# Kernel tuning notes

Hardware: AMD Instinct MI355X
Metric: run time of the kernel (lower is better)

The kernel has to match this reference:

```python
import jax, jax.numpy as jnp
import numpy as np
from jax import lax

B, H, W = 8, 96, 160
CF = 64        # feature channels (= input_channels//2 = out_channels)
OC = 64        # out channels
K = 3          # kernel
G = 8          # deform (offset) groups
PAD, DIL = 1, 1


def conv3x3(x, w, b):
    y = lax.conv_general_dilated(x, w, (1, 1), ((PAD, PAD), (PAD, PAD)),
                                 dimension_numbers=('NCHW', 'OIHW', 'NCHW'))
    return y + b[None, :, None, None]


def lrelu(x):
    return jnp.where(x >= 0, x, 0.1 * x)


def deform_conv2d(x, offset, mask, w, b):
    # x: (B, Cin, H, W); offset: (B, 2*G*K*K, H, W) in (y, x) per tap; mask: (B, G*K*K, H, W)
    Bq, Cin, Hq, Wq = x.shape
    OCq = w.shape[0]
    off = offset.reshape(Bq, G, K, K, 2, Hq, Wq)
    dy, dx = off[:, :, :, :, 0], off[:, :, :, :, 1]        # (B,G,K,K,H,W)
    ky = jnp.arange(K, dtype=x.dtype).reshape(1, 1, K, 1, 1, 1)
    kx = jnp.arange(K, dtype=x.dtype).reshape(1, 1, 1, K, 1, 1)
    hy = jnp.arange(Hq, dtype=x.dtype).reshape(1, 1, 1, 1, Hq, 1)
    wx = jnp.arange(Wq, dtype=x.dtype).reshape(1, 1, 1, 1, 1, Wq)
    ys = dy + hy - PAD + ky * DIL                          # sampling rows
    xs = dx + wx - PAAD if False else dx + wx - PAD + kx * DIL  # sampling cols
    xg = x.reshape(Bq, G, Cin // G, Hq, Wq)

    def sample(img, ysg, xsg):
        # img: (Cg,H,W); ysg/xsg: (K,K,H,W) -> (Cg,K,K,H,W) bilinear with zero padding
        y0 = jnp.floor(ysg)
        x0 = jnp.floor(xsg)
        wy1 = ysg - y0
        wx1 = xsg - x0
        wy0 = 1.0 - wy1
        wx0 = 1.0 - wx1

        def gather(yi, xi):
            valid = ((yi >= 0) & (yi < Hq) & (xi >= 0) & (xi < Wq)).astype(img.dtype)
            yc = jnp.clip(yi, 0, Hq - 1).astype(jnp.int32)
            xc = jnp.clip(xi, 0, Wq - 1).astype(jnp.int32)
            return img[:, yc, xc] * valid[None]

        return (gather(y0, x0) * (wy0 * wx0)[None]
                + gather(y0, x0 + 1) * (wy0 * wx1)[None]
                + gather(y0 + 1, x0) * (wy1 * wx0)[None]
                + gather(y0 + 1, x0 + 1) * (wy1 * wx1)[None])

    sampled = jax.vmap(jax.vmap(sample))(xg, ys, xs)       # (B,G,Cg,K,K,H,W)
    sampled = sampled * mask.reshape(Bq, G, 1, K, K, Hq, Wq)
    wg = w.reshape(OCq, G, Cin // G, K, K)
    return jnp.einsum('bgcijhw,ogcij->bohw', sampled, wg) + b[None, :, None, None]


def setup_inputs() -> dict:
    key = jax.random.key(0)
    ks = jax.random.split(key, 12)
    cin0 = OC * 3 + 4  # 196

    def u(k, shape, fan_in):
        s = 1.0 / np.sqrt(fan_in)
        return jax.random.uniform(k, shape, jnp.float32, -s, s)

    inp = {
        'current_feature_warped': jax.random.normal(ks[0], (B, CF, H, W), jnp.float32),
        'feat_prop': jax.random.normal(ks[1], (B, CF, H, W), jnp.float32),
        'feat_prev': jax.random.normal(ks[2], (B, CF, H, W), jnp.float32),
        'flow1': jax.random.normal(ks[3], (B, 2, H, W), jnp.float32),
        'flow2': jax.random.normal(ks[4], (B, 2, H, W), jnp.float32),
        'w1': u(ks[5], (OC, cin0, 3, 3), cin0 * 9), 'b1': jnp.zeros((OC,), jnp.float32),
        'w2': u(ks[6], (OC, OC, 3, 3), OC * 9), 'b2': jnp.zeros((OC,), jnp.float32),
        'w3': u(ks[7], (OC, OC, 3, 3), OC * 9), 'b3': jnp.zeros((OC,), jnp.float32),
        'w4': u(ks[8], (K * K * 3 * G, OC, 3, 3), OC * 9), 'b4': jnp.zeros((K * K * 3 * G,), jnp.float32),
        'weight': u(ks[9], (OC, CF, 3, 3), 128 * 9),  # init_weights uses n = input_channels*k*k = 128*9
        'bias': jnp.zeros((OC,), jnp.float32),
    }
    return inp

# remove the accidental typo guard (keeps module exec-clean)
PAAD = PAD


def reference(current_feature_warped, feat_prop, feat_prev, flow1, flow2,
              w1, b1, w2, b2, w3, b3, w4, b4, weight, bias):
    cat = jnp.concatenate([current_feature_warped, feat_prop, feat_prev, flow1, flow2], axis=1)
    o = lrelu(conv3x3(cat, w1, b1))
    o = lrelu(conv3x3(o, w2, b2))
    o = lrelu(conv3x3(o, w3, b3))
    o = conv3x3(o, w4, b4)                                  # (B, 3*G*K*K, H, W)
    offset1, offset2, mask = jnp.split(o, 3, axis=1)        # each (B, G*K*K, H, W)
    rep = offset1.shape[1] // 2                             # G*K*K/2 = 36
    offset1 = offset1 + jnp.tile(flow1[:, ::-1], (1, rep, 1, 1))
    offset2 = offset2 + jnp.tile(flow2[:, ::-1], (1, rep, 1, 1))
    offset = jnp.concatenate([offset1, offset2], axis=1)    # (B, 2*G*K*K, H, W)
    mask = jax.nn.sigmoid(mask)
    return deform_conv2d(current_feature_warped, offset, mask, weight, bias)
```

## Files before the change

kernel.cpp:

```cpp
#include <hip/hip_runtime.h>
#include <hip/hip_bf16.h>
#include <math.h>

typedef __attribute__((ext_vector_type(8))) short short8;
typedef __attribute__((ext_vector_type(4))) float f32x4;

constexpr int B_ = 8, H_ = 96, W_ = 160;
constexpr int HW_ = H_ * W_;
constexpr int NPIX = B_ * HW_;

__device__ __forceinline__ unsigned short f2bf(float f) {
    unsigned int u = __builtin_bit_cast(unsigned int, f);
    u += 0x7FFFu + ((u >> 16) & 1u);
    return (unsigned short)(u >> 16);
}
__device__ __forceinline__ float bf2f(unsigned short s) {
    unsigned int u = ((unsigned int)s) << 16;
    return __builtin_bit_cast(float, u);
}
__device__ __forceinline__ unsigned int cvt_pk_bf16(float lo, float hi) {
    unsigned int r;
    asm volatile("v_cvt_pk_bf16_f32 %0, %1, %2" : "=v"(r) : "v"(lo), "v"(hi));
    return r;
}
__device__ __forceinline__ float f4get(const float4& v, int q) {
    switch (q) { case 0: return v.x; case 1: return v.y;
                 case 2: return v.z; default: return v.w; }
}

__global__ __launch_bounds__(256) void prep_x1(
    const float* __restrict__ cfw, const float* __restrict__ fpro,
    const float* __restrict__ fprv, const float* __restrict__ f1,
    const float* __restrict__ f2, unsigned short* __restrict__ X1)
{
    const int c8 = blockIdx.y;
    const int pix0 = blockIdx.x * 1024 + threadIdx.x * 4;
    unsigned short* dst = X1 + ((size_t)c8 * NPIX + pix0) * 8;

    if (c8 >= 25) {
        uint4 z = {0u, 0u, 0u, 0u};
        #pragma unroll
        for (int q = 0; q < 4; ++q) *(uint4*)(dst + q * 8) = z;
        return;
    }

    const int b  = pix0 / HW_;
    const int hw = pix0 - b * HW_;

    float4 v[8];
    #pragma unroll
    for (int j = 0; j < 8; ++j) {
        int c = c8 * 8 + j;
        const float* src = nullptr; int sc = 0, nc = 0;
        if (c < 64)       { src = cfw;  sc = c;       nc = 64; }
        else if (c < 128) { src = fpro; sc = c - 64;  nc = 64; }
        else if (c < 192) { src = fprv; sc = c - 128; nc = 64; }
        else if (c < 194) { src = f1;   sc = c - 192; nc = 2;  }
        else if (c < 196) { src = f2;   sc = c - 194; nc = 2;  }
        if (src) v[j] = *(const float4*)(src + ((size_t)b * nc + sc) * HW_ + hw);
        else     { v[j].x = v[j].y = v[j].z = v[j].w = 0.f; }
    }
    #pragma unroll
    for (int q = 0; q < 4; ++q) {
        uint4 o;
        o.x = cvt_pk_bf16(f4get(v[0], q), f4get(v[1], q));
        o.y = cvt_pk_bf16(f4get(v[2], q), f4get(v[3], q));
        o.z = cvt_pk_bf16(f4get(v[4], q), f4get(v[5], q));
        o.w = cvt_pk_bf16(f4get(v[6], q), f4get(v[7], q));
        *(uint4*)(dst + q * 8) = o;
    }
}

__global__ __launch_bounds__(256) void prep_w(
    const float* __restrict__ w, unsigned short* __restrict__ Bt,
    int Cin, int KCH, int Nout, int NFTOT)
{
    int idx = blockIdx.x * 256 + threadIdx.x;
    int total = 9 * KCH * NFTOT * 64;
    if (idx >= total) return;
    int lane = idx & 63;
    int r = idx >> 6;
    int nf = r % NFTOT; r /= NFTOT;
    int ck = r % KCH;
    int t  = r / KCH;
    int n  = nf * 16 + (lane & 15);
    int kb = ck * 32 + (lane >> 4) * 8;
    short8 o;
    #pragma unroll
    for (int j = 0; j < 8; ++j) {
        int c = kb + j;
        float v = (c < Cin && n < Nout) ? w[((size_t)n * Cin + c) * 9 + t] : 0.f;
        o[j] = (short)f2bf(v);
    }
    *(short8*)(Bt + (size_t)idx * 8) = o;
}

__global__ __launch_bounds__(256) void prep_wd(
    const float* __restrict__ w, unsigned short* __restrict__ Btd)
{
    int idx = blockIdx.x * 256 + threadIdx.x;
    if (idx >= 8 * 3 * 4 * 64) return;
    int lane = idx & 63;
    int r = idx >> 6;
    int nf = r % 4; r >>= 2;
    int ck = r % 3;
    int g  = r / 3;
    int n  = nf * 16 + (lane & 15);
    int kb = ck * 32 + (lane >> 4) * 8;
    short8 o;
    #pragma unroll
    for (int j = 0; j < 8; ++j) {
        int k = kb + j;
        int t = k >> 3, c = k & 7;
        float v = (t < 9) ? w[((size_t)n * 64 + g * 8 + c) * 9 + t] : 0.f;
        o[j] = (short)f2bf(v);
    }
    *(short8*)(Btd + (size_t)idx * 8) = o;
}

template<int KCH, int NFTOT, int NF, bool RELU>
__global__ __launch_bounds__(256) void conv_mfma(
    const unsigned short* __restrict__ X, const unsigned short* __restrict__ Bt,
    const float* __restrict__ bias, unsigned short* __restrict__ Y,
    int CoutTot, int fBase0)
{
    const int lane = threadIdx.x & 63;
    const int wv   = threadIdx.x >> 6;
    const int m0   = blockIdx.x * 128 + wv * 32;
    const int fBase = fBase0 + blockIdx.y * NF;
    const int lm = lane & 15;
    const int l16 = lane >> 4;

    int p[2], hh[2], wp[2];
    #pragma unroll
    for (int mf = 0; mf < 2; ++mf) {
        int pm = m0 + mf * 16 + lm;
        p[mf] = pm;
        hh[mf] = (pm / W_) % H_;
        wp[mf] = pm % W_;
    }

    f32x4 acc[2][NF];
    #pragma unroll
    for (int nf = 0; nf < NF; ++nf) {
        int oc = (fBase + nf) * 16 + lm;
        float bv = (oc < CoutTot) ? bias[oc] : 0.f;
        f32x4 a = {bv, bv, bv, bv};
        acc[0][nf] = a; acc[1][nf] = a;
    }

    const short8 zero = {0,0,0,0,0,0,0,0};

    #pragma unroll
    for (int ck = 0; ck < KCH; ++ck) {
        const int p8 = ck * 4 + l16;
        const unsigned short* Xp = X + (size_t)p8 * NPIX * 8;
        #pragma unroll
        for (int t = 0; t < 9; ++t) {
            const int di = t / 3 - 1, dj = t % 3 - 1;
            const unsigned short* bp =
                Bt + (((size_t)(t * KCH + ck) * NFTOT + fBase) * 64 + lane) * 8;
            short8 bfr[NF];
            #pragma unroll
            for (int nf = 0; nf < NF; ++nf)
                bfr[nf] = *(const short8*)(bp + (size_t)nf * 512);
            #pragma unroll
            for (int mf = 0; mf < 2; ++mf) {
                bool val = ((unsigned)(hh[mf] + di) < (unsigned)H_) &&
                           ((unsigned)(wp[mf] + dj) < (unsigned)W_);
                const unsigned short* ap = Xp + (size_t)(p[mf] + di * W_ + dj) * 8;
                short8 afr = val ? *(const short8*)ap : zero;
                #pragma unroll
                for (int nf = 0; nf < NF; ++nf)
                    acc[mf][nf] = __builtin_amdgcn_mfma_f32_16x16x32_bf16(
                        afr, bfr[nf], acc[mf][nf], 0, 0, 0);
            }
        }
    }

    const int prow = l16 * 4;
    #pragma unroll
    for (int mf = 0; mf < 2; ++mf)
        #pragma unroll
        for (int nf = 0; nf < NF; ++nf) {
            int oc = (fBase + nf) * 16 + lm;
            if (oc < CoutTot) {
                #pragma unroll
                for (int r = 0; r < 4; ++r) {
                    int pix = m0 + mf * 16 + prow + r;
                    float v = acc[mf][nf][r];
                    if (RELU) v = (v >= 0.f) ? v : 0.1f * v;
                    Y[((size_t)(oc >> 3) * NPIX + pix) * 8 + (oc & 7)] = f2bf(v);
                }
            }
        }
}

template<int HALF>
__global__ __launch_bounds__(256, 4) void conv4_mfma(
    const unsigned short* __restrict__ X, const unsigned short* __restrict__ Bt,
    const float* __restrict__ bias,
    unsigned short* __restrict__ oY, unsigned short* __restrict__ oX,
    unsigned short* __restrict__ oM)
{
    const int lane = threadIdx.x & 63;
    const int wv   = threadIdx.x >> 6;
    const int pix0 = blockIdx.x * 128;
    const int m0   = pix0 + wv * 32;
    const int lm = lane & 15;
    const int l16 = lane >> 4;
    constexpr int FB = HALF * 7;

    int p[2], hh[2], wp[2];
    #pragma unroll
    for (int mf = 0; mf < 2; ++mf) {
        int pm = m0 + mf * 16 + lm;
        p[mf] = pm;
        hh[mf] = (pm / W_) % H_;
        wp[mf] = pm % W_;
    }

    f32x4 acc[2][7];
    #pragma unroll
    for (int nf = 0; nf < 7; ++nf) {
        int oc = (FB + nf) * 16 + lm;
        float bv = (oc < 216) ? bias[oc] : 0.f;
        f32x4 a = {bv, bv, bv, bv};
        acc[0][nf] = a; acc[1][nf] = a;
    }

    const short8 zero = {0,0,0,0,0,0,0,0};

    #pragma unroll
    for (int ck = 0; ck < 2; ++ck) {
        const unsigned short* Xp = X + (size_t)(ck * 4 + l16) * NPIX * 8;
        #pragma unroll
        for (int t = 0; t < 9; ++t) {
            const int di = t / 3 - 1, dj = t % 3 - 1;
            const unsigned short* bp =
                Bt + (((size_t)(t * 2 + ck) * 14 + FB) * 64 + lane) * 8;
            short8 afr[2];
            #pragma unroll
            for (int mf = 0; mf < 2; ++mf) {
                bool val = ((unsigned)(hh[mf] + di) < (unsigned)H_) &&
                           ((unsigned)(wp[mf] + dj) < (unsigned)W_);
                const unsigned short* ap = Xp + (size_t)(p[mf] + di * W_ + dj) * 8;
                afr[mf] = val ? *(const short8*)ap : zero;
            }
            #pragma unroll
            for (int nf = 0; nf < 7; ++nf) {
                short8 bfr = *(const short8*)(bp + (size_t)nf * 512);
                acc[0][nf] = __builtin_amdgcn_mfma_f32_16x16x32_bf16(
                    afr[0], bfr, acc[0][nf], 0, 0, 0);
                acc[1][nf] = __builtin_amdgcn_mfma_f32_16x16x32_bf16(
                    afr[1], bfr, acc[1][nf], 0, 0, 0);
            }
        }
    }

    const int prow = l16 * 4;
    #pragma unroll
    for (int mf = 0; mf < 2; ++mf) {
        const int pixb = m0 + mf * 16 + prow;
        #pragma unroll
        for (int nf = 0; nf < 7; ++nf) {
            const int nfg = FB + nf;
            const int oc = nfg * 16 + lm;
            if (nfg < 9) {
                const int pr = nfg * 8 + (lm >> 1);
                unsigned short* plane = ((lm & 1) ? oX : oY) + (size_t)pr * NPIX;
                uint2 sv;
                sv.x = cvt_pk_bf16(acc[mf][nf][0], acc[mf][nf][1]);
                sv.y = cvt_pk_bf16(acc[mf][nf][2], acc[mf][nf][3]);
                *(uint2*)(plane + pixb) = sv;
            } else if (oc < 216) {
                const int mi = (nfg - 9) * 16 + lm;
                float v0 = 1.f / (1.f + expf(-acc[mf][nf][0]));
                float v1 = 1.f / (1.f + expf(-acc[mf][nf][1]));
                float v2 = 1.f / (1.f + expf(-acc[mf][nf][2]));
                float v3 = 1.f / (1.f + expf(-acc[mf][nf][3]));
                uint2 sv;
                sv.x = cvt_pk_bf16(v0, v1);
                sv.y = cvt_pk_bf16(v2, v3);
                *(uint2*)(oM + (size_t)mi * NPIX + pixb) = sv;
            }
        }
    }
}

__global__ __launch_bounds__(256) void deform_mfma(
    const unsigned short* __restrict__ Xg,
    const unsigned short* __restrict__ oY,
    const unsigned short* __restrict__ oX,
    const unsigned short* __restrict__ oM,
    const float* __restrict__ f1, const float* __restrict__ f2,
    const unsigned short* __restrict__ Btd,
    const float* __restrict__ bia,
    float* __restrict__ out)
{
    __shared__ __align__(16) char lds[128 * 65 * 4];
    float* sout = (float*)lds;

    const int tid  = threadIdx.x;
    const int lane = tid & 63;
    const int wv   = tid >> 6;
    const int lm   = lane & 15;
    const int pix0 = blockIdx.x * 128;
    const int b    = pix0 / HW_;
    const int hw0  = pix0 % HW_;

    const int pix = tid & 127;
    const int hi  = tid >> 7;
    const int hw  = hw0 + pix;
    const int h   = hw / W_;
    const int w   = hw - h * W_;
    const size_t gp = (size_t)(pix0 + pix);
    const size_t bF = (size_t)b * 2 * HW_;

    {
        uint4 z = {0u, 0u, 0u, 0u};
        #pragma unroll
        for (int i = 0; i < 8; ++i)
            ((uint4*)lds)[i * 256 + tid] = z;
    }

    f32x4 acc[2][4];
    #pragma unroll
    for (int nf = 0; nf < 4; ++nf) {
        float bv = bia[nf * 16 + lm];
        f32x4 a = {bv, bv, bv, bv};
        acc[0][nf] = a; acc[1][nf] = a;
    }

    for (int g = 0; g < 8; ++g) {
        const unsigned short* Xp = Xg + (size_t)g * NPIX * 8;
        __syncthreads();

        const float* fl = (g < 4) ? f1 : f2;
        const float fy = fl[bF + (size_t)HW_ + hw];
        const float fx = fl[bF + hw];
        unsigned short uy[5], ux[5], um[5];
        #pragma unroll
        for (int it = 0; it < 5; ++it) {
            int t = hi + 2 * it;
            bool act = (it < 4) || (hi == 0);
            if (act) {
                size_t po = (size_t)(g * 9 + t) * NPIX + gp;
                uy[it] = oY[po]; ux[it] = oX[po]; um[it] = oM[po];
            }
        }
        #pragma unroll
        for (int it = 0; it < 5; ++it) {
            int t = hi + 2 * it;
            bool act = (it < 4) || (hi == 0);
            if (act) {
                float dy = bf2f(uy[it]) + fy;
                float dx = bf2f(ux[it]) + fx;
                float m  = bf2f(um[it]);

                float ys = dy + (float)(h - 1 + t / 3);
                float xs = dx + (float)(w - 1 + t % 3);
                float y0f = floorf(ys), x0f = floorf(xs);
                float wy1 = ys - y0f, wx1 = xs - x0f;
                float wy0 = 1.f - wy1, wx0 = 1.f - wx1;
                int iy0 = (int)y0f, ix0 = (int)x0f;
                int iy1 = iy0 + 1,  ix1 = ix0 + 1;
                bool vy0 = (unsigned)iy0 < (unsigned)H_;
                bool vy1 = (unsigned)iy1 < (unsigned)H_;
                bool vx0 = (unsigned)ix0 < (unsigned)W_;
                bool vx1 = (unsigned)ix1 < (unsigned)W_;
                int cy0 = min(max(iy0, 0), H_ - 1), cy1 = min(max(iy1, 0), H_ - 1);
                int cx0 = min(max(ix0, 0), W_ - 1), cx1 = min(max(ix1, 0), W_ - 1);
                float w00 = (vy0 && vx0) ? wy0 * wx0 * m : 0.f;
                float w01 = (vy0 && vx1) ? wy0 * wx1 * m : 0.f;
                float w10 = (vy1 && vx0) ? wy1 * wx0 * m : 0.f;
                float w11 = (vy1 && vx1) ? wy1 * wx1 * m : 0.f;

                size_t r0 = (size_t)b * HW_ + (size_t)cy0 * W_;
                size_t r1 = (size_t)b * HW_ + (size_t)cy1 * W_;
                uint4 c00 = *(const uint4*)(Xp + (r0 + cx0) * 8);
                uint4 c01 = *(const uint4*)(Xp + (r0 + cx1) * 8);
                uint4 c10 = *(const uint4*)(Xp + (r1 + cx0) * 8);
                uint4 c11 = *(const uint4*)(Xp + (r1 + cx1) * 8);

                float a8[8];
                #pragma unroll
                for (int i = 0; i < 8; ++i) a8[i] = 0.f;
                const unsigned int u00[4] = {c00.x, c00.y, c00.z, c00.w};
                const unsigned int u01[4] = {c01.x, c01.y, c01.z, c01.w};
                const unsigned int u10[4] = {c10.x, c10.y, c10.z, c10.w};
                const unsigned int u11[4] = {c11.x, c11.y, c11.z, c11.w};
                #pragma unroll
                for (int i = 0; i < 4; ++i) {
                    a8[2*i]   += w00 * __builtin_bit_cast(float, u00[i] << 16);
                    a8[2*i+1] += w00 * __builtin_bit_cast(float, u00[i] & 0xFFFF0000u);
                    a8[2*i]   += w01 * __builtin_bit_cast(float, u01[i] << 16);
                    a8[2*i+1] += w01 * __builtin_bit_cast(float, u01[i] & 0xFFFF0000u);
                    a8[2*i]   += w10 * __builtin_bit_cast(float, u10[i] << 16);
                    a8[2*i+1] += w10 * __builtin_bit_cast(float, u10[i] & 0xFFFF0000u);
                    a8[2*i]   += w11 * __builtin_bit_cast(float, u11[i] << 16);
                    a8[2*i+1] += w11 * __builtin_bit_cast(float, u11[i] & 0xFFFF0000u);
                }
                uint4 ov;
                ov.x = cvt_pk_bf16(a8[0], a8[1]);
                ov.y = cvt_pk_bf16(a8[2], a8[3]);
                ov.z = cvt_pk_bf16(a8[4], a8[5]);
                ov.w = cvt_pk_bf16(a8[6], a8[7]);
                int slot = t ^ (pix & 7);
                *(uint4*)(lds + pix * 256 + slot * 16) = ov;
            }
        }
        __syncthreads();
        #pragma unroll
        for (int ck = 0; ck < 3; ++ck) {
            const short8* bpp = (const short8*)Btd + ((size_t)(g * 3 + ck) * 4) * 64 + lane;
            short8 bfr[4];
            #pragma unroll
            for (int nf = 0; nf < 4; ++nf) bfr[nf] = bpp[nf * 64];
            const int slotbase = ck * 4 + (lane >> 4);
            #pragma unroll
            for (int mf = 0; mf < 2; ++mf) {
                int row = wv * 32 + mf * 16 + lm;
                int slot = slotbase ^ (lm & 7);
                short8 afr = *(const short8*)(lds + row * 256 + slot * 16);
                #pragma unroll
                for (int nf = 0; nf < 4; ++nf)
                    acc[mf][nf] = __builtin_amdgcn_mfma_f32_16x16x32_bf16(
                        afr, bfr[nf], acc[mf][nf], 0, 0, 0);
            }
        }
    }

    __syncthreads();
    const int prow = (lane >> 4) * 4;
    #pragma unroll
    for (int mf = 0; mf < 2; ++mf)
        #pragma unroll
        for (int nf = 0; nf < 4; ++nf)
            #pragma unroll
            for (int r = 0; r < 4; ++r)
                sout[(wv * 32 + mf * 16 + prow + r) * 65 + nf * 16 + lm] = acc[mf][nf][r];
    __syncthreads();
    #pragma unroll
    for (int i = 0; i < 32; ++i) {
        int idx = i * 256 + tid;
        int oc = idx >> 7;
        int pp = idx & 127;
        out[((size_t)(b * 64 + oc)) * HW_ + hw0 + pp] = sout[pp * 65 + oc];
    }
}

extern "C" void kernel_launch(void* const* d_in, const int* in_sizes, int n_in,
                              void* d_out, int out_size, void* d_ws, size_t ws_size,
                              hipStream_t stream)
{
    const float* cfw  = (const float*)d_in[0];
    const float* fpro = (const float*)d_in[1];
    const float* fprv = (const float*)d_in[2];
    const float* fl1  = (const float*)d_in[3];
    const float* fl2  = (const float*)d_in[4];
    const float* w1   = (const float*)d_in[5];
    const float* b1   = (const float*)d_in[6];
    const float* w2   = (const float*)d_in[7];
    const float* b2   = (const float*)d_in[8];
    const float* w3   = (const float*)d_in[9];
    const float* b3   = (const float*)d_in[10];
    const float* w4   = (const float*)d_in[11];
    const float* b4   = (const float*)d_in[12];
    const float* wdef = (const float*)d_in[13];
    const float* bdef = (const float*)d_in[14];
    float* out = (float*)d_out;

    char* ws = (char*)d_ws;
    unsigned short* X1  = (unsigned short*)(ws);
    unsigned short* buf1= (unsigned short*)(ws + 55050240);
    unsigned short* o2  = (unsigned short*)(ws + 70778880);
    unsigned short* oY  = (unsigned short*)(ws + 70778880);
    unsigned short* oX  = oY + (size_t)72 * NPIX;
    unsigned short* oM  = oX + (size_t)72 * NPIX;
    unsigned short* Bt1 = (unsigned short*)(ws + 125829120);
    unsigned short* Bt2 = (unsigned short*)(ws + 125829120 + 258048);
    unsigned short* Bt3 = (unsigned short*)(ws + 125829120 + 258048 + 73728);
    unsigned short* Bt4 = (unsigned short*)(ws + 125829120 + 258048 + 2*73728);
    unsigned short* Btd = (unsigned short*)(ws + 125829120 + 2*258048 + 2*73728);

    prep_x1<<<dim3(NPIX / 1024, 28), dim3(256), 0, stream>>>(
        cfw, fpro, fprv, fl1, fl2, X1);
    prep_w<<<dim3((9*7*4*64 + 255) / 256), dim3(256), 0, stream>>>(w1, Bt1, 196, 7, 64, 4);
    prep_w<<<dim3((9*2*4*64 + 255) / 256), dim3(256), 0, stream>>>(w2, Bt2, 64, 2, 64, 4);
    prep_w<<<dim3((9*2*4*64 + 255) / 256), dim3(256), 0, stream>>>(w3, Bt3, 64, 2, 64, 4);
    prep_w<<<dim3((9*2*14*64 + 255) / 256), dim3(256), 0, stream>>>(w4, Bt4, 64, 2, 216, 14);
    prep_wd<<<dim3((8*3*4*64 + 255) / 256), dim3(256), 0, stream>>>(wdef, Btd);

    dim3 blk(256);
    dim3 gridM(NPIX / 128, 1);
    conv_mfma<7, 4, 4, true><<<gridM, blk, 0, stream>>>(X1, Bt1, b1, buf1, 64, 0);
    conv_mfma<2, 4, 4, true><<<gridM, blk, 0, stream>>>(buf1, Bt2, b2, o2, 64, 0);
    conv_mfma<2, 4, 4, true><<<gridM, blk, 0, stream>>>(o2, Bt3, b3, buf1, 64, 0);
    conv4_mfma<0><<<gridM, blk, 0, stream>>>(buf1, Bt4, b4, oY, oX, oM);
    conv4_mfma<1><<<gridM, blk, 0, stream>>>(buf1, Bt4, b4, oY, oX, oM);
    deform_mfma<<<dim3(NPIX / 128), blk, 0, stream>>>(
        X1, oY, oX, oM, fl1, fl2, Btd, bdef, out);
}
```

Measured before the change: 280.8 us.

## Stage conv weights through LDS with register prefetch and prefetch deform offsets

The conv_mfma and conv4_mfma kernels now load each tap's weight fragment cooperatively into shared memory, one 16-byte chunk per thread. The next tap's chunk is prefetched into registers while the current one is consumed. Before this, every wave fetched the same weights from global memory on its own. The deform kernel hoists the flow loads out of the group loop and software-pipelines the offset/mask loads one group ahead. The cost is two barriers per tap step and extra registers.

```diff
diff --git a/kernel.cpp b/kernel.cpp
--- a/kernel.cpp
+++ b/kernel.cpp
@@ -124,8 +124,12 @@
     const float* __restrict__ bias, unsigned short* __restrict__ Y,
     int CoutTot, int fBase0)
 {
-    const int lane = threadIdx.x & 63;
-    const int wv   = threadIdx.x >> 6;
+    static_assert(NF == 4, "staging assumes 4 KB step chunk");
+    __shared__ __align__(16) unsigned short bsh[NF * 512];
+
+    const int tid  = threadIdx.x;
+    const int lane = tid & 63;
+    const int wv   = tid >> 6;
     const int m0   = blockIdx.x * 128 + wv * 32;
     const int fBase = fBase0 + blockIdx.y * NF;
     const int lm = lane & 15;
@@ -150,31 +154,37 @@
     }
 
     const short8 zero = {0,0,0,0,0,0,0,0};
-
-    #pragma unroll
-    for (int ck = 0; ck < KCH; ++ck) {
-        const int p8 = ck * 4 + l16;
-        const unsigned short* Xp = X + (size_t)p8 * NPIX * 8;
-        #pragma unroll
-        for (int t = 0; t < 9; ++t) {
-            const int di = t / 3 - 1, dj = t % 3 - 1;
-            const unsigned short* bp =
-                Bt + (((size_t)(t * KCH + ck) * NFTOT + fBase) * 64 + lane) * 8;
-            short8 bfr[NF];
+    constexpr int S = KCH * 9;
+
+    uint4 bt = *(const uint4*)(Bt + (size_t)fBase * 512 + tid * 8);
+
+    #pragma unroll
+    for (int s = 0; s < S; ++s) {
+        const int ck = s / 9, t = s % 9;
+        __syncthreads();
+        *(uint4*)(bsh + tid * 8) = bt;
+        __syncthreads();
+        if (s + 1 < S) {
+            const int ck2 = (s + 1) / 9, t2 = (s + 1) % 9;
+            bt = *(const uint4*)(Bt +
+                ((size_t)(t2 * KCH + ck2) * NFTOT + fBase) * 512 + tid * 8);
+        }
+        const int di = t / 3 - 1, dj = t % 3 - 1;
+        const unsigned short* Xp = X + (size_t)(ck * 4 + l16) * NPIX * 8;
+        short8 bfr[NF];
+        #pragma unroll
+        for (int nf = 0; nf < NF; ++nf)
+            bfr[nf] = *(const short8*)(bsh + nf * 512 + lane * 8);
+        #pragma unroll
+        for (int mf = 0; mf < 2; ++mf) {
+            bool val = ((unsigned)(hh[mf] + di) < (unsigned)H_) &&
+                       ((unsigned)(wp[mf] + dj) < (unsigned)W_);
+            const unsigned short* ap = Xp + (size_t)(p[mf] + di * W_ + dj) * 8;
+            short8 afr = val ? *(const short8*)ap : zero;
             #pragma unroll
             for (int nf = 0; nf < NF; ++nf)
-                bfr[nf] = *(const short8*)(bp + (size_t)nf * 512);
-            #pragma unroll
-            for (int mf = 0; mf < 2; ++mf) {
-                bool val = ((unsigned)(hh[mf] + di) < (unsigned)H_) &&
-                           ((unsigned)(wp[mf] + dj) < (unsigned)W_);
-                const unsigned short* ap = Xp + (size_t)(p[mf] + di * W_ + dj) * 8;
-                short8 afr = val ? *(const short8*)ap : zero;
-                #pragma unroll
-                for (int nf = 0; nf < NF; ++nf)
-                    acc[mf][nf] = __builtin_amdgcn_mfma_f32_16x16x32_bf16(
-                        afr, bfr[nf], acc[mf][nf], 0, 0, 0);
-            }
+                acc[mf][nf] = __builtin_amdgcn_mfma_f32_16x16x32_bf16(
+                    afr, bfr[nf], acc[mf][nf], 0, 0, 0);
         }
     }
 
@@ -203,8 +213,11 @@
     unsigned short* __restrict__ oY, unsigned short* __restrict__ oX,
     unsigned short* __restrict__ oM)
 {
-    const int lane = threadIdx.x & 63;
-    const int wv   = threadIdx.x >> 6;
+    __shared__ __align__(16) unsigned short bsh[7 * 512];
+
+    const int tid  = threadIdx.x;
+    const int lane = tid & 63;
+    const int wv   = tid >> 6;
     const int pix0 = blockIdx.x * 128;
     const int m0   = pix0 + wv * 32;
     const int lm = lane & 15;
@@ -230,31 +243,43 @@
     }
 
     const short8 zero = {0,0,0,0,0,0,0,0};
-
-    #pragma unroll
-    for (int ck = 0; ck < 2; ++ck) {
+    const bool two = (tid < 192);
+
+    uint4 bt0 = *(const uint4*)(Bt + (size_t)FB * 512 + tid * 8);
+    uint4 bt1 = {0u, 0u, 0u, 0u};
+    if (two) bt1 = *(const uint4*)(Bt + (size_t)FB * 512 + (256 + tid) * 8);
+
+    #pragma unroll
+    for (int s = 0; s < 18; ++s) {
+        const int ck = s / 9, t = s % 9;
+        __syncthreads();
+        *(uint4*)(bsh + tid * 8) = bt0;
+        if (two) *(uint4*)(bsh + (256 + tid) * 8) = bt1;
+        __syncthreads();
+        if (s + 1 < 18) {
+            const int ck2 = (s + 1) / 9, t2 = (s + 1) % 9;
+            const unsigned short* nb =
+                Bt + ((size_t)((t2 * 2 + ck2) * 14 + FB)) * 512;
+            bt0 = *(const uint4*)(nb + tid * 8);
+            if (two) bt1 = *(const uint4*)(nb + (256 + tid) * 8);
+        }
+        const int di = t / 3 - 1, dj = t % 3 - 1;
         const unsigned short* Xp = X + (size_t)(ck * 4 + l16) * NPIX * 8;
-        #pragma unroll
-        for (int t = 0; t < 9; ++t) {
-            const int di = t / 3 - 1, dj = t % 3 - 1;
-            const unsigned short* bp =
-                Bt + (((size_t)(t * 2 + ck) * 14 + FB) * 64 + lane) * 8;
-            short8 afr[2];
-            #pragma unroll
-            for (int mf = 0; mf < 2; ++mf) {
-                bool val = ((unsigned)(hh[mf] + di) < (unsigned)H_) &&
-                           ((unsigned)(wp[mf] + dj) < (unsigned)W_);
-                const unsigned short* ap = Xp + (size_t)(p[mf] + di * W_ + dj) * 8;
-                afr[mf] = val ? *(const short8*)ap : zero;
-            }
-            #pragma unroll
-            for (int nf = 0; nf < 7; ++nf) {
-                short8 bfr = *(const short8*)(bp + (size_t)nf * 512);
-                acc[0][nf] = __builtin_amdgcn_mfma_f32_16x16x32_bf16(
-                    afr[0], bfr, acc[0][nf], 0, 0, 0);
-                acc[1][nf] = __builtin_amdgcn_mfma_f32_16x16x32_bf16(
-                    afr[1], bfr, acc[1][nf], 0, 0, 0);
-            }
+        short8 afr[2];
+        #pragma unroll
+        for (int mf = 0; mf < 2; ++mf) {
+            bool val = ((unsigned)(hh[mf] + di) < (unsigned)H_) &&
+                       ((unsigned)(wp[mf] + dj) < (unsigned)W_);
+            const unsigned short* ap = Xp + (size_t)(p[mf] + di * W_ + dj) * 8;
+            afr[mf] = val ? *(const short8*)ap : zero;
+        }
+        #pragma unroll
+        for (int nf = 0; nf < 7; ++nf) {
+            short8 bfr = *(const short8*)(bsh + nf * 512 + lane * 8);
+            acc[0][nf] = __builtin_amdgcn_mfma_f32_16x16x32_bf16(
+                afr[0], bfr, acc[0][nf], 0, 0, 0);
+            acc[1][nf] = __builtin_amdgcn_mfma_f32_16x16x32_bf16(
+                afr[1], bfr, acc[1][nf], 0, 0, 0);
         }
     }
 
@@ -317,6 +342,9 @@
     const size_t gp = (size_t)(pix0 + pix);
     const size_t bF = (size_t)b * 2 * HW_;
 
+    const float fy1 = f1[bF + (size_t)HW_ + hw], fx1 = f1[bF + hw];
+    const float fy2 = f2[bF + (size_t)HW_ + hw], fx2 = f2[bF + hw];
+
     {
         uint4 z = {0u, 0u, 0u, 0u};
         #pragma unroll
@@ -332,23 +360,35 @@
         acc[0][nf] = a; acc[1][nf] = a;
     }
 
+    unsigned short uy[5], ux[5], um[5];
+    #pragma unroll
+    for (int it = 0; it < 5; ++it) {
+        int t = hi + 2 * it;
+        if ((it < 4) || (hi == 0)) {
+            size_t po = (size_t)t * NPIX + gp;
+            uy[it] = oY[po]; ux[it] = oX[po]; um[it] = oM[po];
+        }
+    }
+
     for (int g = 0; g < 8; ++g) {
         const unsigned short* Xp = Xg + (size_t)g * NPIX * 8;
+        const float fy = (g < 4) ? fy1 : fy2;
+        const float fx = (g < 4) ? fx1 : fx2;
+
         __syncthreads();
 
-        const float* fl = (g < 4) ? f1 : f2;
-        const float fy = fl[bF + (size_t)HW_ + hw];
-        const float fx = fl[bF + hw];
-        unsigned short uy[5], ux[5], um[5];
-        #pragma unroll
-        for (int it = 0; it < 5; ++it) {
-            int t = hi + 2 * it;
-            bool act = (it < 4) || (hi == 0);
-            if (act) {
-                size_t po = (size_t)(g * 9 + t) * NPIX + gp;
-                uy[it] = oY[po]; ux[it] = oX[po]; um[it] = oM[po];
+        unsigned short nuy[5], nux[5], num[5];
+        if (g < 7) {
+            #pragma unroll
+            for (int it = 0; it < 5; ++it) {
+                int t = hi + 2 * it;
+                if ((it < 4) || (hi == 0)) {
+                    size_t po = (size_t)((g + 1) * 9 + t) * NPIX + gp;
+                    nuy[it] = oY[po]; nux[it] = oX[po]; num[it] = oM[po];
+                }
             }
         }
+
         #pragma unroll
         for (int it = 0; it < 5; ++it) {
             int t = hi + 2 * it;
@@ -429,6 +469,12 @@
                         afr, bfr[nf], acc[mf][nf], 0, 0, 0);
             }
         }
+        if (g < 7) {
+            #pragma unroll
+            for (int it = 0; it < 5; ++it) {
+                uy[it] = nuy[it]; ux[it] = nux[it]; um[it] = num[it];
+            }
+        }
     }
 
     __syncthreads();
```

New measurement: 286.4 us. 1.02x slower.
